# Kernel tuning notes

Measured on AMD Instinct MI355X. Metric: run time of the kernel, lower is better.

The kernel has to match this reference:

```python
import jax, jax.numpy as jnp
import numpy as np


def setup_inputs() -> dict:
    key = jax.random.key(0)
    k1, k2, k3, k4, k5 = jax.random.split(key, 5)
    B, S, D_IN, D_OUT = 4, 2048, 4096, 4096
    x = jax.random.normal(k1, (B, S, D_IN), dtype=jnp.float32)
    q_weight = jax.random.randint(k2, (D_OUT, D_IN), 0, 256, dtype=jnp.int32)
    scale = jax.random.uniform(k3, (), dtype=jnp.float32) * 0.01 + 1e-4
    zero_point = jnp.round(jax.random.uniform(k4, (), dtype=jnp.float32) * 255.0)
    bias = jax.random.normal(k5, (D_OUT,), dtype=jnp.float32)
    return {"x": x, "q_weight": q_weight, "scale": scale,
            "zero_point": zero_point, "bias": bias}


def reference(x, q_weight, scale, zero_point, bias):
    # Dequantize: w = scale * (q - zero_point), per-tensor scalar scale/zp.
    weight = scale * (q_weight.astype(jnp.float32) - zero_point)  # [out, in]
    # F.linear: y = x @ w.T + b
    return jnp.einsum('bsi,oi->bso', x, weight) + bias
```

## Files before the change

kernel.cpp:

```cpp
#include <hip/hip_runtime.h>
#include <hip/hip_bf16.h>


typedef __attribute__((ext_vector_type(8))) __bf16 bf16x8;
typedef __attribute__((ext_vector_type(4))) float f32x4;
typedef __attribute__((ext_vector_type(4))) int i32x4;
typedef __attribute__((ext_vector_type(8))) unsigned short u16x8;

#define M_DIM 8192
#define N_DIM 4096
#define K_DIM 4096
#define BM 256
#define BN 256
#define BK 64
#define NT (K_DIM / BK)

#define MFMA16(A, B, C) __builtin_amdgcn_mfma_f32_16x16x32_bf16(A, B, C, 0, 0, 0)

__device__ __forceinline__ unsigned short f2bf(float f) {
  __hip_bfloat16 h = __float2bfloat16(f);
  unsigned short u;
  __builtin_memcpy(&u, &h, 2);
  return u;
}

__global__ __launch_bounds__(256) void cvt_x_kernel(const float* __restrict__ x,
                                                    unsigned short* __restrict__ out) {
  size_t i = (size_t)blockIdx.x * 256 + threadIdx.x;
  f32x4 a = ((const f32x4*)x)[2 * i];
  f32x4 b = ((const f32x4*)x)[2 * i + 1];
  u16x8 o;
  o[0] = f2bf(a[0]); o[1] = f2bf(a[1]); o[2] = f2bf(a[2]); o[3] = f2bf(a[3]);
  o[4] = f2bf(b[0]); o[5] = f2bf(b[1]); o[6] = f2bf(b[2]); o[7] = f2bf(b[3]);
  *(u16x8*)(out + 8 * i) = o;
}

__global__ __launch_bounds__(256) void cvt_w_kernel(const int* __restrict__ q,
                                                    const float* __restrict__ zp_ptr,
                                                    unsigned short* __restrict__ out) {
  const float zp = *zp_ptr;
  size_t i = (size_t)blockIdx.x * 256 + threadIdx.x;
  i32x4 a = ((const i32x4*)q)[2 * i];
  i32x4 b = ((const i32x4*)q)[2 * i + 1];
  u16x8 o;
  o[0] = f2bf((float)a[0] - zp); o[1] = f2bf((float)a[1] - zp);
  o[2] = f2bf((float)a[2] - zp); o[3] = f2bf((float)a[3] - zp);
  o[4] = f2bf((float)b[0] - zp); o[5] = f2bf((float)b[1] - zp);
  o[6] = f2bf((float)b[2] - zp); o[7] = f2bf((float)b[3] - zp);
  *(u16x8*)(out + 8 * i) = o;
}

__device__ __forceinline__ bf16x8 lds_frag(const char* base, int row, int ks, int lh) {
  int byte = row * 128 + ks * 64 + lh * 16;
  byte ^= ((byte >> 7) & 7) << 4;
  return *(const bf16x8*)(base + byte);
}

__device__ __forceinline__ void stage_half(const unsigned short* __restrict__ g,
                                           size_t grow0, int k0, char* lds,
                                           int tileOff, int h, int w, int lane) {
#pragma unroll
  for (int j = 0; j < 2; ++j) {
    const int chunk = (w * 2 + j) * 1024;
    const int d = h * 16384 + chunk + lane * 16;
    const int sd = d ^ (((d >> 7) & 7) << 4);
    const int row = sd >> 7;
    const int colB = sd & 127;
    const char* src = (const char*)g + ((grow0 + row) * (size_t)K_DIM + k0) * 2 + colB;
    __builtin_amdgcn_global_load_lds(
        (const __attribute__((address_space(1))) void*)src,
        (__attribute__((address_space(3))) void*)(lds + tileOff + h * 16384 + chunk),
        16, 0, 0);
  }
}

__global__ __launch_bounds__(512, 2) void gemm8_kernel(
    const unsigned short* __restrict__ A, const unsigned short* __restrict__ B,
    const float* __restrict__ scale_ptr, const float* __restrict__ bias,
    float* __restrict__ C) {
  __shared__ __align__(16) char lds[131072];

  const int t = threadIdx.x;
  const int lane = t & 63;
  const int w = t >> 6;
  const int wm = w >> 2;
  const int wn = w & 3;
  const int ll = lane & 15;
  const int lh = lane >> 4;

  const int nwg = gridDim.x * gridDim.y;
  const int flat = blockIdx.y * gridDim.x + blockIdx.x;
  const int per = nwg >> 3;
  const int sw = (flat & 7) * per + (flat >> 3);
  const int tn = sw & (N_DIM / BN - 1);
  const int tm = sw / (N_DIM / BN);
  const size_t gm0 = (size_t)tm * BM;
  const size_t gn0 = (size_t)tn * BN;

  f32x4 acc[8][4] = {};

  stage_half(A, gm0, 0, lds, 0, 0, w, lane);
  stage_half(A, gm0, 0, lds, 0, 1, w, lane);
  stage_half(B, gn0, 0, lds, 32768, 0, w, lane);
  stage_half(B, gn0, 0, lds, 32768, 1, w, lane);
  stage_half(B, gn0, BK, lds, 65536 + 32768, 0, w, lane);
  stage_half(B, gn0, BK, lds, 65536 + 32768, 1, w, lane);
  stage_half(A, gm0, BK, lds, 65536, 0, w, lane);
  asm volatile("s_waitcnt vmcnt(6)" ::: "memory");
  __builtin_amdgcn_s_barrier();

#pragma unroll 2
  for (int T = 0; T < NT; ++T) {
    const int c = T & 1;
    const int aOff = c * 65536;
    const int bOff = c * 65536 + 32768;

    bf16x8 a[4][2], b0[2][2], b1[2][2];

#pragma unroll
    for (int fi = 0; fi < 4; ++fi)
#pragma unroll
      for (int ks = 0; ks < 2; ++ks)
        a[fi][ks] = lds_frag(&lds[aOff], wm * 128 + fi * 16 + ll, ks, lh);
#pragma unroll
    for (int fj = 0; fj < 2; ++fj)
#pragma unroll
      for (int ks = 0; ks < 2; ++ks)
        b0[fj][ks] = lds_frag(&lds[bOff], wn * 64 + fj * 16 + ll, ks, lh);
    if (T < NT - 1)
      stage_half(A, gm0, (T + 1) * BK, lds, (c ^ 1) * 65536, 1, w, lane);
    __builtin_amdgcn_s_barrier();
    __builtin_amdgcn_s_setprio(1);
#pragma unroll
    for (int fi = 0; fi < 4; ++fi)
#pragma unroll
      for (int fj = 0; fj < 2; ++fj) {
        acc[fi][fj] = MFMA16(a[fi][0], b0[fj][0], acc[fi][fj]);
        acc[fi][fj] = MFMA16(a[fi][1], b0[fj][1], acc[fi][fj]);
      }
    __builtin_amdgcn_s_setprio(0);
    asm volatile("s_waitcnt lgkmcnt(0)" ::: "memory");
    __builtin_amdgcn_s_barrier();

#pragma unroll
    for (int fj = 0; fj < 2; ++fj)
#pragma unroll
      for (int ks = 0; ks < 2; ++ks)
        b1[fj][ks] = lds_frag(&lds[bOff], wn * 64 + 32 + fj * 16 + ll, ks, lh);
    __builtin_amdgcn_s_barrier();
    __builtin_amdgcn_s_setprio(1);
#pragma unroll
    for (int fi = 0; fi < 4; ++fi)
#pragma unroll
      for (int fj = 0; fj < 2; ++fj) {
        acc[fi][2 + fj] = MFMA16(a[fi][0], b1[fj][0], acc[fi][2 + fj]);
        acc[fi][2 + fj] = MFMA16(a[fi][1], b1[fj][1], acc[fi][2 + fj]);
      }
    __builtin_amdgcn_s_setprio(0);
    asm volatile("s_waitcnt lgkmcnt(0)" ::: "memory");
    __builtin_amdgcn_s_barrier();

#pragma unroll
    for (int fi = 0; fi < 4; ++fi)
#pragma unroll
      for (int ks = 0; ks < 2; ++ks)
        a[fi][ks] = lds_frag(&lds[aOff], wm * 128 + 64 + fi * 16 + ll, ks, lh);
    if (T < NT - 2)
      stage_half(B, gn0, (T + 2) * BK, lds, bOff, 0, w, lane);
    __builtin_amdgcn_s_barrier();
    __builtin_amdgcn_s_setprio(1);
#pragma unroll
    for (int fi = 0; fi < 4; ++fi)
#pragma unroll
      for (int fj = 0; fj < 2; ++fj) {
        acc[4 + fi][2 + fj] = MFMA16(a[fi][0], b1[fj][0], acc[4 + fi][2 + fj]);
        acc[4 + fi][2 + fj] = MFMA16(a[fi][1], b1[fj][1], acc[4 + fi][2 + fj]);
      }
    __builtin_amdgcn_s_setprio(0);
    asm volatile("s_waitcnt lgkmcnt(0)" ::: "memory");
    __builtin_amdgcn_s_barrier();

    if (T < NT - 2) {
      stage_half(B, gn0, (T + 2) * BK, lds, bOff, 1, w, lane);
      stage_half(A, gm0, (T + 2) * BK, lds, aOff, 0, w, lane);
    }
    __builtin_amdgcn_s_barrier();
    __builtin_amdgcn_s_setprio(1);
#pragma unroll
    for (int fi = 0; fi < 4; ++fi)
#pragma unroll
      for (int fj = 0; fj < 2; ++fj) {
        acc[4 + fi][fj] = MFMA16(a[fi][0], b0[fj][0], acc[4 + fi][fj]);
        acc[4 + fi][fj] = MFMA16(a[fi][1], b0[fj][1], acc[4 + fi][fj]);
      }
    __builtin_amdgcn_s_setprio(0);
    if (T < NT - 2) {
      asm volatile("s_waitcnt vmcnt(6)" ::: "memory");
    } else {
      asm volatile("s_waitcnt vmcnt(0)" ::: "memory");
    }
    __builtin_amdgcn_s_barrier();
  }

  const float sc = *scale_ptr;
#pragma unroll
  for (int nh = 0; nh < 2; ++nh)
#pragma unroll
    for (int fj = 0; fj < 2; ++fj) {
      const size_t col = gn0 + wn * 64 + nh * 32 + fj * 16 + ll;
      const float bv = bias[col];
#pragma unroll
      for (int mh = 0; mh < 2; ++mh)
#pragma unroll
        for (int fi = 0; fi < 4; ++fi) {
          const size_t row0 = gm0 + wm * 128 + mh * 64 + fi * 16 + lh * 4;
          const f32x4 v = acc[mh * 4 + fi][nh * 2 + fj];
#pragma unroll
          for (int r = 0; r < 4; ++r)
            C[(row0 + r) * N_DIM + col] = sc * v[r] + bv;
        }
    }
}

__global__ __launch_bounds__(256, 2) void gemm_fallback_kernel(
    const float* __restrict__ Aptr, const int* __restrict__ Wptr,
    const float* __restrict__ scale_ptr, const float* __restrict__ zp_ptr,
    const float* __restrict__ bias, float* __restrict__ C) {
  __shared__ unsigned short As[128 * 32];
  __shared__ unsigned short Ws[128 * 32];
  const int t = threadIdx.x;
  const int lane = t & 63;
  const int w = t >> 6;
  const int wm = w >> 1, wn = w & 1;
  const size_t gm0 = (size_t)blockIdx.y * 128;
  const size_t gn0 = (size_t)blockIdx.x * 128;
  f32x4 acc[4][4] = {};
  const float zp = *zp_ptr;
  for (int k0 = 0; k0 < K_DIM; k0 += 32) {
    __syncthreads();
    const int row = t >> 1;
    const int kh = (t & 1) * 16;
    const float* sa = Aptr + (gm0 + row) * (size_t)K_DIM + k0 + kh;
    f32x4 a0 = ((const f32x4*)sa)[0], a1 = ((const f32x4*)sa)[1];
    f32x4 a2 = ((const f32x4*)sa)[2], a3 = ((const f32x4*)sa)[3];
    u16x8 o0, o1;
    o0[0] = f2bf(a0[0]); o0[1] = f2bf(a0[1]); o0[2] = f2bf(a0[2]); o0[3] = f2bf(a0[3]);
    o0[4] = f2bf(a1[0]); o0[5] = f2bf(a1[1]); o0[6] = f2bf(a1[2]); o0[7] = f2bf(a1[3]);
    o1[0] = f2bf(a2[0]); o1[1] = f2bf(a2[1]); o1[2] = f2bf(a2[2]); o1[3] = f2bf(a2[3]);
    o1[4] = f2bf(a3[0]); o1[5] = f2bf(a3[1]); o1[6] = f2bf(a3[2]); o1[7] = f2bf(a3[3]);
    *(u16x8*)&As[row * 32 + kh] = o0;
    *(u16x8*)&As[row * 32 + kh + 8] = o1;
    const int* sw = Wptr + (gn0 + row) * (size_t)K_DIM + k0 + kh;
    i32x4 w0 = ((const i32x4*)sw)[0], w1 = ((const i32x4*)sw)[1];
    i32x4 w2 = ((const i32x4*)sw)[2], w3 = ((const i32x4*)sw)[3];
    u16x8 p0, p1;
    p0[0] = f2bf((float)w0[0] - zp); p0[1] = f2bf((float)w0[1] - zp);
    p0[2] = f2bf((float)w0[2] - zp); p0[3] = f2bf((float)w0[3] - zp);
    p0[4] = f2bf((float)w1[0] - zp); p0[5] = f2bf((float)w1[1] - zp);
    p0[6] = f2bf((float)w1[2] - zp); p0[7] = f2bf((float)w1[3] - zp);
    p1[0] = f2bf((float)w2[0] - zp); p1[1] = f2bf((float)w2[1] - zp);
    p1[2] = f2bf((float)w2[2] - zp); p1[3] = f2bf((float)w2[3] - zp);
    p1[4] = f2bf((float)w3[0] - zp); p1[5] = f2bf((float)w3[1] - zp);
    p1[6] = f2bf((float)w3[2] - zp); p1[7] = f2bf((float)w3[3] - zp);
    *(u16x8*)&Ws[row * 32 + kh] = p0;
    *(u16x8*)&Ws[row * 32 + kh + 8] = p1;
    __syncthreads();
    bf16x8 af[4], bfr[4];
#pragma unroll
    for (int f = 0; f < 4; ++f) {
      af[f] = *(const bf16x8*)&As[(wm * 64 + f * 16 + (lane & 15)) * 32 + (lane >> 4) * 8];
      bfr[f] = *(const bf16x8*)&Ws[(wn * 64 + f * 16 + (lane & 15)) * 32 + (lane >> 4) * 8];
    }
#pragma unroll
    for (int i = 0; i < 4; ++i)
#pragma unroll
      for (int j = 0; j < 4; ++j)
        acc[i][j] = MFMA16(af[i], bfr[j], acc[i][j]);
  }
  const float sc = *scale_ptr;
#pragma unroll
  for (int i = 0; i < 4; ++i) {
    const int rbase = wm * 64 + i * 16 + ((lane >> 4) << 2);
#pragma unroll
    for (int j = 0; j < 4; ++j) {
      const size_t col = gn0 + wn * 64 + j * 16 + (lane & 15);
      const float bv = bias[col];
#pragma unroll
      for (int r = 0; r < 4; ++r)
        C[(gm0 + rbase + r) * N_DIM + col] = sc * acc[i][j][r] + bv;
    }
  }
}

extern "C" void kernel_launch(void* const* d_in, const int* in_sizes, int n_in,
                              void* d_out, int out_size, void* d_ws, size_t ws_size,
                              hipStream_t stream) {
  const float* x = (const float*)d_in[0];
  const int* q = (const int*)d_in[1];
  const float* scale = (const float*)d_in[2];
  const float* zp = (const float*)d_in[3];
  const float* bias = (const float*)d_in[4];
  float* out = (float*)d_out;

  const size_t needA = (size_t)M_DIM * K_DIM * 2;
  const size_t needW = (size_t)N_DIM * K_DIM * 2;

  if (ws_size >= needA + needW) {
    unsigned short* Abf = (unsigned short*)d_ws;
    unsigned short* Wbf = (unsigned short*)((char*)d_ws + needA);
    cvt_x_kernel<<<(M_DIM * (size_t)K_DIM) / (8 * 256), 256, 0, stream>>>(x, Abf);
    cvt_w_kernel<<<(N_DIM * (size_t)K_DIM) / (8 * 256), 256, 0, stream>>>(q, zp, Wbf);
    dim3 grid(N_DIM / BN, M_DIM / BM);
    gemm8_kernel<<<grid, 512, 0, stream>>>(Abf, Wbf, scale, bias, out);
  } else {
    dim3 grid(N_DIM / 128, M_DIM / 128);
    gemm_fallback_kernel<<<grid, 256, 0, stream>>>(x, q, scale, zp, bias, out);
  }
}
```

Baseline: 292.7 us.

## Merge per-phase barrier pairs into single wait-then-barrier sync points

Replaces the two barriers per MFMA phase with one combined sync point: a vmcnt wait, one s_barrier, an lgkmcnt wait and a sched_barrier, placed before each compute block. The end-of-phase barriers and the trailing vmcnt wait are removed, and the outstanding-load counts are redistributed across phases. The goal is to halve barrier stalls in the main K loop. The risk is LDS read/write hazards or incorrect vmcnt thresholds, and the sched_barrier may limit the compiler's ability to interleave instructions.

```diff
diff --git a/kernel.cpp b/kernel.cpp
--- a/kernel.cpp
+++ b/kernel.cpp
@@ -74,6 +74,24 @@
   }
 }
 
+#define PHASE_SYNC(VM)                                         \
+  do {                                                         \
+    if (T < NT - 2)                                            \
+      asm volatile("s_waitcnt vmcnt(" #VM ")" ::: "memory");   \
+    else                                                       \
+      asm volatile("s_waitcnt vmcnt(0)" ::: "memory");         \
+    __builtin_amdgcn_s_barrier();                              \
+    asm volatile("s_waitcnt lgkmcnt(0)" ::: "memory");         \
+    __builtin_amdgcn_sched_barrier(0);                         \
+  } while (0)
+
+#define PHASE_SYNC_NOVM()                                      \
+  do {                                                         \
+    __builtin_amdgcn_s_barrier();                              \
+    asm volatile("s_waitcnt lgkmcnt(0)" ::: "memory");         \
+    __builtin_amdgcn_sched_barrier(0);                         \
+  } while (0)
+
 __global__ __launch_bounds__(512, 2) void gemm8_kernel(
     const unsigned short* __restrict__ A, const unsigned short* __restrict__ B,
     const float* __restrict__ scale_ptr, const float* __restrict__ bias,
@@ -129,7 +147,7 @@
         b0[fj][ks] = lds_frag(&lds[bOff], wn * 64 + fj * 16 + ll, ks, lh);
     if (T < NT - 1)
       stage_half(A, gm0, (T + 1) * BK, lds, (c ^ 1) * 65536, 1, w, lane);
-    __builtin_amdgcn_s_barrier();
+    PHASE_SYNC(10);
     __builtin_amdgcn_s_setprio(1);
 #pragma unroll
     for (int fi = 0; fi < 4; ++fi)
@@ -139,15 +157,13 @@
         acc[fi][fj] = MFMA16(a[fi][1], b0[fj][1], acc[fi][fj]);
       }
     __builtin_amdgcn_s_setprio(0);
-    asm volatile("s_waitcnt lgkmcnt(0)" ::: "memory");
-    __builtin_amdgcn_s_barrier();
 
 #pragma unroll
     for (int fj = 0; fj < 2; ++fj)
 #pragma unroll
       for (int ks = 0; ks < 2; ++ks)
         b1[fj][ks] = lds_frag(&lds[bOff], wn * 64 + 32 + fj * 16 + ll, ks, lh);
-    __builtin_amdgcn_s_barrier();
+    PHASE_SYNC(8);
     __builtin_amdgcn_s_setprio(1);
 #pragma unroll
     for (int fi = 0; fi < 4; ++fi)
@@ -157,8 +173,6 @@
         acc[fi][2 + fj] = MFMA16(a[fi][1], b1[fj][1], acc[fi][2 + fj]);
       }
     __builtin_amdgcn_s_setprio(0);
-    asm volatile("s_waitcnt lgkmcnt(0)" ::: "memory");
-    __builtin_amdgcn_s_barrier();
 
 #pragma unroll
     for (int fi = 0; fi < 4; ++fi)
@@ -167,7 +181,7 @@
         a[fi][ks] = lds_frag(&lds[aOff], wm * 128 + 64 + fi * 16 + ll, ks, lh);
     if (T < NT - 2)
       stage_half(B, gn0, (T + 2) * BK, lds, bOff, 0, w, lane);
-    __builtin_amdgcn_s_barrier();
+    PHASE_SYNC_NOVM();
     __builtin_amdgcn_s_setprio(1);
 #pragma unroll
     for (int fi = 0; fi < 4; ++fi)
@@ -177,14 +191,12 @@
         acc[4 + fi][2 + fj] = MFMA16(a[fi][1], b1[fj][1], acc[4 + fi][2 + fj]);
       }
     __builtin_amdgcn_s_setprio(0);
-    asm volatile("s_waitcnt lgkmcnt(0)" ::: "memory");
-    __builtin_amdgcn_s_barrier();
 
     if (T < NT - 2) {
       stage_half(B, gn0, (T + 2) * BK, lds, bOff, 1, w, lane);
       stage_half(A, gm0, (T + 2) * BK, lds, aOff, 0, w, lane);
     }
-    __builtin_amdgcn_s_barrier();
+    PHASE_SYNC(8);
     __builtin_amdgcn_s_setprio(1);
 #pragma unroll
     for (int fi = 0; fi < 4; ++fi)
@@ -194,12 +206,6 @@
         acc[4 + fi][fj] = MFMA16(a[fi][1], b0[fj][1], acc[4 + fi][fj]);
       }
     __builtin_amdgcn_s_setprio(0);
-    if (T < NT - 2) {
-      asm volatile("s_waitcnt vmcnt(6)" ::: "memory");
-    } else {
-      asm volatile("s_waitcnt vmcnt(0)" ::: "memory");
-    }
-    __builtin_amdgcn_s_barrier();
   }
 
   const float sc = *scale_ptr;
```

New measurement: 281.6 us. -3.8%, faster.

## Software-pipeline LDS fragment loads across K iterations with explicit register double-buffering

Applied to the files above, without the earlier changes.

Restructures the main GEMM loop so the A and B fragments for the next K tile are read from LDS during the current tile's MFMA phases. It uses separate a0/a1 and b0/b1 register sets, prefetches the first fragments before the loop, and reorders the quadrant MFMA sequence. Several explicit lgkmcnt waits and barriers are removed, and the global-load stage and vmcnt wait points are moved around. The aim is to hide LDS latency behind matrix-core work, at the cost of more registers and a harder-to-verify ordering between LDS buffer reuse and barriers.

```diff
diff --git a/kernel.cpp b/kernel.cpp
--- a/kernel.cpp
+++ b/kernel.cpp
@@ -98,108 +98,115 @@
   const size_t gn0 = (size_t)tn * BN;
 
   f32x4 acc[8][4] = {};
+  bf16x8 a0[4][2], a1[4][2], b0[2][2], b1[2][2];
 
   stage_half(A, gm0, 0, lds, 0, 0, w, lane);
   stage_half(A, gm0, 0, lds, 0, 1, w, lane);
   stage_half(B, gn0, 0, lds, 32768, 0, w, lane);
   stage_half(B, gn0, 0, lds, 32768, 1, w, lane);
+  asm volatile("s_waitcnt vmcnt(0)" ::: "memory");
+  __builtin_amdgcn_s_barrier();
+#pragma unroll
+  for (int fi = 0; fi < 4; ++fi)
+#pragma unroll
+    for (int ks = 0; ks < 2; ++ks)
+      a0[fi][ks] = lds_frag(&lds[0], wm * 128 + fi * 16 + ll, ks, lh);
+#pragma unroll
+  for (int fj = 0; fj < 2; ++fj)
+#pragma unroll
+    for (int ks = 0; ks < 2; ++ks)
+      b0[fj][ks] = lds_frag(&lds[32768], wn * 64 + fj * 16 + ll, ks, lh);
   stage_half(B, gn0, BK, lds, 65536 + 32768, 0, w, lane);
   stage_half(B, gn0, BK, lds, 65536 + 32768, 1, w, lane);
   stage_half(A, gm0, BK, lds, 65536, 0, w, lane);
-  asm volatile("s_waitcnt vmcnt(6)" ::: "memory");
-  __builtin_amdgcn_s_barrier();
 
 #pragma unroll 2
   for (int T = 0; T < NT; ++T) {
     const int c = T & 1;
     const int aOff = c * 65536;
-    const int bOff = c * 65536 + 32768;
-
-    bf16x8 a[4][2], b0[2][2], b1[2][2];
-
-#pragma unroll
-    for (int fi = 0; fi < 4; ++fi)
+    const int bOff = aOff + 32768;
+    const int aN = (c ^ 1) * 65536;
+    const int bN = aN + 32768;
+
+    __builtin_amdgcn_s_barrier();
+#pragma unroll
+    for (int fj = 0; fj < 2; ++fj)
 #pragma unroll
       for (int ks = 0; ks < 2; ++ks)
-        a[fi][ks] = lds_frag(&lds[aOff], wm * 128 + fi * 16 + ll, ks, lh);
-#pragma unroll
-    for (int fj = 0; fj < 2; ++fj)
-#pragma unroll
-      for (int ks = 0; ks < 2; ++ks)
-        b0[fj][ks] = lds_frag(&lds[bOff], wn * 64 + fj * 16 + ll, ks, lh);
-    if (T < NT - 1)
-      stage_half(A, gm0, (T + 1) * BK, lds, (c ^ 1) * 65536, 1, w, lane);
-    __builtin_amdgcn_s_barrier();
+        b1[fj][ks] = lds_frag(&lds[bOff], wn * 64 + 32 + fj * 16 + ll, ks, lh);
     __builtin_amdgcn_s_setprio(1);
 #pragma unroll
     for (int fi = 0; fi < 4; ++fi)
 #pragma unroll
       for (int fj = 0; fj < 2; ++fj) {
-        acc[fi][fj] = MFMA16(a[fi][0], b0[fj][0], acc[fi][fj]);
-        acc[fi][fj] = MFMA16(a[fi][1], b0[fj][1], acc[fi][fj]);
+        acc[fi][fj] = MFMA16(a0[fi][0], b0[fj][0], acc[fi][fj]);
+        acc[fi][fj] = MFMA16(a0[fi][1], b0[fj][1], acc[fi][fj]);
       }
     __builtin_amdgcn_s_setprio(0);
-    asm volatile("s_waitcnt lgkmcnt(0)" ::: "memory");
+    if (T < NT - 1)
+      stage_half(A, gm0, (T + 1) * BK, lds, aN, 1, w, lane);
+
     __builtin_amdgcn_s_barrier();
-
-#pragma unroll
-    for (int fj = 0; fj < 2; ++fj)
+#pragma unroll
+    for (int fi = 0; fi < 4; ++fi)
 #pragma unroll
       for (int ks = 0; ks < 2; ++ks)
-        b1[fj][ks] = lds_frag(&lds[bOff], wn * 64 + 32 + fj * 16 + ll, ks, lh);
-    __builtin_amdgcn_s_barrier();
+        a1[fi][ks] = lds_frag(&lds[aOff], wm * 128 + 64 + fi * 16 + ll, ks, lh);
     __builtin_amdgcn_s_setprio(1);
 #pragma unroll
     for (int fi = 0; fi < 4; ++fi)
 #pragma unroll
       for (int fj = 0; fj < 2; ++fj) {
-        acc[fi][2 + fj] = MFMA16(a[fi][0], b1[fj][0], acc[fi][2 + fj]);
-        acc[fi][2 + fj] = MFMA16(a[fi][1], b1[fj][1], acc[fi][2 + fj]);
+        acc[fi][2 + fj] = MFMA16(a0[fi][0], b1[fj][0], acc[fi][2 + fj]);
+        acc[fi][2 + fj] = MFMA16(a0[fi][1], b1[fj][1], acc[fi][2 + fj]);
       }
     __builtin_amdgcn_s_setprio(0);
-    asm volatile("s_waitcnt lgkmcnt(0)" ::: "memory");
-    __builtin_amdgcn_s_barrier();
-
-#pragma unroll
-    for (int fi = 0; fi < 4; ++fi)
-#pragma unroll
-      for (int ks = 0; ks < 2; ++ks)
-        a[fi][ks] = lds_frag(&lds[aOff], wm * 128 + 64 + fi * 16 + ll, ks, lh);
     if (T < NT - 2)
       stage_half(B, gn0, (T + 2) * BK, lds, bOff, 0, w, lane);
+
     __builtin_amdgcn_s_barrier();
+    if (T < NT - 2)
+      asm volatile("s_waitcnt vmcnt(2)" ::: "memory");
+    else
+      asm volatile("s_waitcnt vmcnt(0)" ::: "memory");
+    if (T < NT - 1) {
+#pragma unroll
+      for (int fi = 0; fi < 4; ++fi)
+#pragma unroll
+        for (int ks = 0; ks < 2; ++ks)
+          a0[fi][ks] = lds_frag(&lds[aN], wm * 128 + fi * 16 + ll, ks, lh);
+    }
     __builtin_amdgcn_s_setprio(1);
 #pragma unroll
     for (int fi = 0; fi < 4; ++fi)
 #pragma unroll
       for (int fj = 0; fj < 2; ++fj) {
-        acc[4 + fi][2 + fj] = MFMA16(a[fi][0], b1[fj][0], acc[4 + fi][2 + fj]);
-        acc[4 + fi][2 + fj] = MFMA16(a[fi][1], b1[fj][1], acc[4 + fi][2 + fj]);
+        acc[4 + fi][fj] = MFMA16(a1[fi][0], b0[fj][0], acc[4 + fi][fj]);
+        acc[4 + fi][fj] = MFMA16(a1[fi][1], b0[fj][1], acc[4 + fi][fj]);
       }
     __builtin_amdgcn_s_setprio(0);
-    asm volatile("s_waitcnt lgkmcnt(0)" ::: "memory");
+    if (T < NT - 2)
+      stage_half(B, gn0, (T + 2) * BK, lds, bOff, 1, w, lane);
+
     __builtin_amdgcn_s_barrier();
-
-    if (T < NT - 2) {
-      stage_half(B, gn0, (T + 2) * BK, lds, bOff, 1, w, lane);
-      stage_half(A, gm0, (T + 2) * BK, lds, aOff, 0, w, lane);
-    }
-    __builtin_amdgcn_s_barrier();
+    if (T < NT - 1) {
+#pragma unroll
+      for (int fj = 0; fj < 2; ++fj)
+#pragma unroll
+        for (int ks = 0; ks < 2; ++ks)
+          b0[fj][ks] = lds_frag(&lds[bN], wn * 64 + fj * 16 + ll, ks, lh);
+    }
     __builtin_amdgcn_s_setprio(1);
 #pragma unroll
     for (int fi = 0; fi < 4; ++fi)
 #pragma unroll
       for (int fj = 0; fj < 2; ++fj) {
-        acc[4 + fi][fj] = MFMA16(a[fi][0], b0[fj][0], acc[4 + fi][fj]);
-        acc[4 + fi][fj] = MFMA16(a[fi][1], b0[fj][1], acc[4 + fi][fj]);
+        acc[4 + fi][2 + fj] = MFMA16(a1[fi][0], b1[fj][0], acc[4 + fi][2 + fj]);
+        acc[4 + fi][2 + fj] = MFMA16(a1[fi][1], b1[fj][1], acc[4 + fi][2 + fj]);
       }
     __builtin_amdgcn_s_setprio(0);
-    if (T < NT - 2) {
-      asm volatile("s_waitcnt vmcnt(6)" ::: "memory");
-    } else {
-      asm volatile("s_waitcnt vmcnt(0)" ::: "memory");
-    }
-    __builtin_amdgcn_s_barrier();
+    if (T < NT - 2)
+      stage_half(A, gm0, (T + 2) * BK, lds, aOff, 0, w, lane);
   }
 
   const float sc = *scale_ptr;
```

Result: slower. 513.6 us (+75.4%).

## Precompute LDS/global addresses and replace lgkmcnt waits with vmcnt-staged barriers

Applied to the files above, without the earlier changes.

Rewrites the GEMM main loop as an explicitly double-unrolled ktile routine. LDS fragment pointers and global source pointers are precomputed once, which removes per-iteration swizzle and address arithmetic. The per-phase s_waitcnt lgkmcnt(0) plus double-barrier pattern becomes one barrier per phase with finer vmcnt waits, so there are fewer synchronisation points. This risks races if the vmcnt counts or the removed lgkmcnt waits do not match the in-flight loads.

```diff
diff --git a/kernel.cpp b/kernel.cpp
--- a/kernel.cpp
+++ b/kernel.cpp
@@ -50,28 +50,105 @@
   *(u16x8*)(out + 8 * i) = o;
 }
 
-__device__ __forceinline__ bf16x8 lds_frag(const char* base, int row, int ks, int lh) {
-  int byte = row * 128 + ks * 64 + lh * 16;
-  byte ^= ((byte >> 7) & 7) << 4;
-  return *(const bf16x8*)(base + byte);
-}
-
-__device__ __forceinline__ void stage_half(const unsigned short* __restrict__ g,
-                                           size_t grow0, int k0, char* lds,
-                                           int tileOff, int h, int w, int lane) {
-#pragma unroll
-  for (int j = 0; j < 2; ++j) {
-    const int chunk = (w * 2 + j) * 1024;
-    const int d = h * 16384 + chunk + lane * 16;
-    const int sd = d ^ (((d >> 7) & 7) << 4);
-    const int row = sd >> 7;
-    const int colB = sd & 127;
-    const char* src = (const char*)g + ((grow0 + row) * (size_t)K_DIM + k0) * 2 + colB;
-    __builtin_amdgcn_global_load_lds(
-        (const __attribute__((address_space(1))) void*)src,
-        (__attribute__((address_space(3))) void*)(lds + tileOff + h * 16384 + chunk),
-        16, 0, 0);
-  }
+__device__ __forceinline__ void stage2(const char* s0, const char* s1, char* ldsT,
+                                       int h, int Ti, int chunk0, int chunk1) {
+  const size_t off = (size_t)Ti * 128 + (size_t)h * 1048576;
+  __builtin_amdgcn_global_load_lds(
+      (const __attribute__((address_space(1))) void*)(s0 + off),
+      (__attribute__((address_space(3))) void*)(ldsT + h * 16384 + chunk0), 16, 0, 0);
+  __builtin_amdgcn_global_load_lds(
+      (const __attribute__((address_space(1))) void*)(s1 + off),
+      (__attribute__((address_space(3))) void*)(ldsT + h * 16384 + chunk1), 16, 0, 0);
+}
+
+#define FENCE() asm volatile("" ::: "memory")
+
+__device__ __forceinline__ void ktile(
+    int T, const char* pak0, const char* pak1, const char* pbk0, const char* pbk1,
+    char* curA, char* curB, char* nxtA,
+    const char* srcA0, const char* srcA1, const char* srcB0, const char* srcB1,
+    int chunk0, int chunk1, f32x4 (&acc)[8][4]) {
+  bf16x8 af[4][2], b0f[2][2], b1f[2][2];
+
+#pragma unroll
+  for (int fi = 0; fi < 4; ++fi) {
+    af[fi][0] = *(const bf16x8*)(pak0 + fi * 2048);
+    af[fi][1] = *(const bf16x8*)(pak1 + fi * 2048);
+  }
+#pragma unroll
+  for (int fj = 0; fj < 2; ++fj) {
+    b0f[fj][0] = *(const bf16x8*)(pbk0 + fj * 2048);
+    b0f[fj][1] = *(const bf16x8*)(pbk1 + fj * 2048);
+  }
+  if (T < NT - 1) stage2(srcA0, srcA1, nxtA, 1, T + 1, chunk0, chunk1);
+  if (T < NT - 2) asm volatile("s_waitcnt vmcnt(10)" ::: "memory");
+  else            asm volatile("s_waitcnt vmcnt(0)" ::: "memory");
+  __builtin_amdgcn_s_barrier();
+  FENCE();
+  __builtin_amdgcn_s_setprio(1);
+#pragma unroll
+  for (int fi = 0; fi < 4; ++fi)
+#pragma unroll
+    for (int fj = 0; fj < 2; ++fj) {
+      acc[fi][fj] = MFMA16(af[fi][0], b0f[fj][0], acc[fi][fj]);
+      acc[fi][fj] = MFMA16(af[fi][1], b0f[fj][1], acc[fi][fj]);
+    }
+  __builtin_amdgcn_s_setprio(0);
+
+#pragma unroll
+  for (int fj = 0; fj < 2; ++fj) {
+    b1f[fj][0] = *(const bf16x8*)(pbk0 + 4096 + fj * 2048);
+    b1f[fj][1] = *(const bf16x8*)(pbk1 + 4096 + fj * 2048);
+  }
+  if (T < NT - 2) asm volatile("s_waitcnt vmcnt(8)" ::: "memory");
+  else            asm volatile("s_waitcnt vmcnt(0)" ::: "memory");
+  __builtin_amdgcn_s_barrier();
+  FENCE();
+  __builtin_amdgcn_s_setprio(1);
+#pragma unroll
+  for (int fi = 0; fi < 4; ++fi)
+#pragma unroll
+    for (int fj = 0; fj < 2; ++fj) {
+      acc[fi][2 + fj] = MFMA16(af[fi][0], b1f[fj][0], acc[fi][2 + fj]);
+      acc[fi][2 + fj] = MFMA16(af[fi][1], b1f[fj][1], acc[fi][2 + fj]);
+    }
+  __builtin_amdgcn_s_setprio(0);
+
+#pragma unroll
+  for (int fi = 0; fi < 4; ++fi) {
+    af[fi][0] = *(const bf16x8*)(pak0 + 8192 + fi * 2048);
+    af[fi][1] = *(const bf16x8*)(pak1 + 8192 + fi * 2048);
+  }
+  if (T < NT - 2) stage2(srcB0, srcB1, curB, 0, T + 2, chunk0, chunk1);
+  __builtin_amdgcn_s_barrier();
+  FENCE();
+  __builtin_amdgcn_s_setprio(1);
+#pragma unroll
+  for (int fi = 0; fi < 4; ++fi)
+#pragma unroll
+    for (int fj = 0; fj < 2; ++fj) {
+      acc[4 + fi][2 + fj] = MFMA16(af[fi][0], b1f[fj][0], acc[4 + fi][2 + fj]);
+      acc[4 + fi][2 + fj] = MFMA16(af[fi][1], b1f[fj][1], acc[4 + fi][2 + fj]);
+    }
+  __builtin_amdgcn_s_setprio(0);
+
+  if (T < NT - 2) {
+    stage2(srcB0, srcB1, curB, 1, T + 2, chunk0, chunk1);
+    stage2(srcA0, srcA1, curA, 0, T + 2, chunk0, chunk1);
+  }
+  if (T < NT - 2) asm volatile("s_waitcnt vmcnt(8)" ::: "memory");
+  else            asm volatile("s_waitcnt vmcnt(0)" ::: "memory");
+  __builtin_amdgcn_s_barrier();
+  FENCE();
+  __builtin_amdgcn_s_setprio(1);
+#pragma unroll
+  for (int fi = 0; fi < 4; ++fi)
+#pragma unroll
+    for (int fj = 0; fj < 2; ++fj) {
+      acc[4 + fi][fj] = MFMA16(af[fi][0], b0f[fj][0], acc[4 + fi][fj]);
+      acc[4 + fi][fj] = MFMA16(af[fi][1], b0f[fj][1], acc[4 + fi][fj]);
+    }
+  __builtin_amdgcn_s_setprio(0);
 }
 
 __global__ __launch_bounds__(512, 2) void gemm8_kernel(
@@ -97,109 +174,49 @@
   const size_t gm0 = (size_t)tm * BM;
   const size_t gn0 = (size_t)tn * BN;
 
+  char* lA0 = (char*)lds;
+  char* lB0 = (char*)lds + 32768;
+  char* lA1 = (char*)lds + 65536;
+  char* lB1 = (char*)lds + 98304;
+
+  const int sbase = (lh * 16) ^ ((ll & 7) << 4);
+  const char* pa0k0 = lA0 + wm * 16384 + ll * 128 + sbase;
+  const char* pa0k1 = lA0 + wm * 16384 + ll * 128 + (sbase ^ 64);
+  const char* pb0k0 = lB0 + wn * 8192 + ll * 128 + sbase;
+  const char* pb0k1 = lB0 + wn * 8192 + ll * 128 + (sbase ^ 64);
+  const char* pa1k0 = pa0k0 + 65536;
+  const char* pa1k1 = pa0k1 + 65536;
+  const char* pb1k0 = pb0k0 + 65536;
+  const char* pb1k1 = pb0k1 + 65536;
+
+  const int rowS0 = w * 16 + (lane >> 3);
+  const int rowS1 = w * 16 + 8 + (lane >> 3);
+  const int colSB = ((lane & 7) * 16) ^ (((lane >> 3) & 7) << 4);
+  const int chunk0 = w * 2048;
+  const int chunk1 = w * 2048 + 1024;
+  const char* srcA0 = (const char*)A + (gm0 + rowS0) * (size_t)(K_DIM * 2) + colSB;
+  const char* srcA1 = (const char*)A + (gm0 + rowS1) * (size_t)(K_DIM * 2) + colSB;
+  const char* srcB0 = (const char*)B + (gn0 + rowS0) * (size_t)(K_DIM * 2) + colSB;
+  const char* srcB1 = (const char*)B + (gn0 + rowS1) * (size_t)(K_DIM * 2) + colSB;
+
   f32x4 acc[8][4] = {};
 
-  stage_half(A, gm0, 0, lds, 0, 0, w, lane);
-  stage_half(A, gm0, 0, lds, 0, 1, w, lane);
-  stage_half(B, gn0, 0, lds, 32768, 0, w, lane);
-  stage_half(B, gn0, 0, lds, 32768, 1, w, lane);
-  stage_half(B, gn0, BK, lds, 65536 + 32768, 0, w, lane);
-  stage_half(B, gn0, BK, lds, 65536 + 32768, 1, w, lane);
-  stage_half(A, gm0, BK, lds, 65536, 0, w, lane);
+  stage2(srcA0, srcA1, lA0, 0, 0, chunk0, chunk1);
+  stage2(srcA0, srcA1, lA0, 1, 0, chunk0, chunk1);
+  stage2(srcB0, srcB1, lB0, 0, 0, chunk0, chunk1);
+  stage2(srcB0, srcB1, lB0, 1, 0, chunk0, chunk1);
+  stage2(srcB0, srcB1, lB1, 0, 1, chunk0, chunk1);
+  stage2(srcB0, srcB1, lB1, 1, 1, chunk0, chunk1);
+  stage2(srcA0, srcA1, lA1, 0, 1, chunk0, chunk1);
   asm volatile("s_waitcnt vmcnt(6)" ::: "memory");
   __builtin_amdgcn_s_barrier();
-
-#pragma unroll 2
-  for (int T = 0; T < NT; ++T) {
-    const int c = T & 1;
-    const int aOff = c * 65536;
-    const int bOff = c * 65536 + 32768;
-
-    bf16x8 a[4][2], b0[2][2], b1[2][2];
-
-#pragma unroll
-    for (int fi = 0; fi < 4; ++fi)
-#pragma unroll
-      for (int ks = 0; ks < 2; ++ks)
-        a[fi][ks] = lds_frag(&lds[aOff], wm * 128 + fi * 16 + ll, ks, lh);
-#pragma unroll
-    for (int fj = 0; fj < 2; ++fj)
-#pragma unroll
-      for (int ks = 0; ks < 2; ++ks)
-        b0[fj][ks] = lds_frag(&lds[bOff], wn * 64 + fj * 16 + ll, ks, lh);
-    if (T < NT - 1)
-      stage_half(A, gm0, (T + 1) * BK, lds, (c ^ 1) * 65536, 1, w, lane);
-    __builtin_amdgcn_s_barrier();
-    __builtin_amdgcn_s_setprio(1);
-#pragma unroll
-    for (int fi = 0; fi < 4; ++fi)
-#pragma unroll
-      for (int fj = 0; fj < 2; ++fj) {
-        acc[fi][fj] = MFMA16(a[fi][0], b0[fj][0], acc[fi][fj]);
-        acc[fi][fj] = MFMA16(a[fi][1], b0[fj][1], acc[fi][fj]);
-      }
-    __builtin_amdgcn_s_setprio(0);
-    asm volatile("s_waitcnt lgkmcnt(0)" ::: "memory");
-    __builtin_amdgcn_s_barrier();
-
-#pragma unroll
-    for (int fj = 0; fj < 2; ++fj)
-#pragma unroll
-      for (int ks = 0; ks < 2; ++ks)
-        b1[fj][ks] = lds_frag(&lds[bOff], wn * 64 + 32 + fj * 16 + ll, ks, lh);
-    __builtin_amdgcn_s_barrier();
-    __builtin_amdgcn_s_setprio(1);
-#pragma unroll
-    for (int fi = 0; fi < 4; ++fi)
-#pragma unroll
-      for (int fj = 0; fj < 2; ++fj) {
-        acc[fi][2 + fj] = MFMA16(a[fi][0], b1[fj][0], acc[fi][2 + fj]);
-        acc[fi][2 + fj] = MFMA16(a[fi][1], b1[fj][1], acc[fi][2 + fj]);
-      }
-    __builtin_amdgcn_s_setprio(0);
-    asm volatile("s_waitcnt lgkmcnt(0)" ::: "memory");
-    __builtin_amdgcn_s_barrier();
-
-#pragma unroll
-    for (int fi = 0; fi < 4; ++fi)
-#pragma unroll
-      for (int ks = 0; ks < 2; ++ks)
-        a[fi][ks] = lds_frag(&lds[aOff], wm * 128 + 64 + fi * 16 + ll, ks, lh);
-    if (T < NT - 2)
-      stage_half(B, gn0, (T + 2) * BK, lds, bOff, 0, w, lane);
-    __builtin_amdgcn_s_barrier();
-    __builtin_amdgcn_s_setprio(1);
-#pragma unroll
-    for (int fi = 0; fi < 4; ++fi)
-#pragma unroll
-      for (int fj = 0; fj < 2; ++fj) {
-        acc[4 + fi][2 + fj] = MFMA16(a[fi][0], b1[fj][0], acc[4 + fi][2 + fj]);
-        acc[4 + fi][2 + fj] = MFMA16(a[fi][1], b1[fj][1], acc[4 + fi][2 + fj]);
-      }
-    __builtin_amdgcn_s_setprio(0);
-    asm volatile("s_waitcnt lgkmcnt(0)" ::: "memory");
-    __builtin_amdgcn_s_barrier();
-
-    if (T < NT - 2) {
-      stage_half(B, gn0, (T + 2) * BK, lds, bOff, 1, w, lane);
-      stage_half(A, gm0, (T + 2) * BK, lds, aOff, 0, w, lane);
-    }
-    __builtin_amdgcn_s_barrier();
-    __builtin_amdgcn_s_setprio(1);
-#pragma unroll
-    for (int fi = 0; fi < 4; ++fi)
-#pragma unroll
-      for (int fj = 0; fj < 2; ++fj) {
-        acc[4 + fi][fj] = MFMA16(a[fi][0], b0[fj][0], acc[4 + fi][fj]);
-        acc[4 + fi][fj] = MFMA16(a[fi][1], b0[fj][1], acc[4 + fi][fj]);
-      }
-    __builtin_amdgcn_s_setprio(0);
-    if (T < NT - 2) {
-      asm volatile("s_waitcnt vmcnt(6)" ::: "memory");
-    } else {
-      asm volatile("s_waitcnt vmcnt(0)" ::: "memory");
-    }
-    __builtin_amdgcn_s_barrier();
+  FENCE();
+
+  for (int T2 = 0; T2 < NT; T2 += 2) {
+    ktile(T2, pa0k0, pa0k1, pb0k0, pb0k1, lA0, lB0, lA1,
+          srcA0, srcA1, srcB0, srcB1, chunk0, chunk1, acc);
+    ktile(T2 + 1, pa1k0, pa1k1, pb1k0, pb1k1, lA1, lB1, lA0,
+          srcA0, srcA1, srcB0, srcB1, chunk0, chunk1, acc);
   }
 
   const float sc = *scale_ptr;
```

Measured after the change: 283.0 us. 1.03x faster.
